# Kernel tuning notes

Hardware: AMD Instinct MI355X
Metric: run time of the kernel (lower is better)

## Reference

```python
import jax, jax.numpy as jnp
import numpy as np

B, R, N, K, E = 128, 500, 500, 10, 128
H1 = 5 * E  # UnvisitedMLP hidden = embedding_dim * 5


def setup_inputs() -> dict:
    key = jax.random.key(0)
    ks = jax.random.split(key, 8)
    current = jax.random.randint(ks[0], (B, R), 0, N)
    distance = jax.random.uniform(ks[1], (B, N, N), dtype=jnp.float32)
    # unvisited cities, exercising the padding-index path in search_unvisited.
    visited = jax.random.uniform(ks[2], (B, R, N)) < 0.97
    masked = jnp.where(visited, -jnp.inf, 0.0).astype(jnp.float32)
    encoded_nodes = jax.random.normal(ks[3], (B, N, E), dtype=jnp.float32)
    w1 = jax.random.normal(ks[4], (H1, K * E), dtype=jnp.float32) * (1.0 / np.sqrt(K * E))
    b1 = jnp.zeros((H1,), dtype=jnp.float32)
    w2 = jax.random.normal(ks[5], (E, H1), dtype=jnp.float32) * (1.0 / np.sqrt(H1))
    b2 = jnp.zeros((E,), dtype=jnp.float32)
    return {"current": current, "distance": distance, "masked": masked,
            "encoded_nodes": encoded_nodes, "w1": w1, "b1": b1, "w2": w2, "b2": b2}


def _search_unvisited(current, distance, masked, k_near):
    # distance_filtered[b, r, :] = distance[b, current[b, r], :]  -> [B, R, N]
    b_idx = jnp.arange(current.shape[0])[:, None]
    distance_filtered = distance[b_idx, current, :]
    mask_unvisited = masked != -jnp.inf
    distance_masked = jnp.where(mask_unvisited, distance_filtered, jnp.inf)
    # k smallest == top-k of negated distances
    neg_vals, k_idx = jax.lax.top_k(-distance_masked, k_near)  # [B, R, K]
    is_inf = neg_vals == -jnp.inf  # entries that were +inf (no unvisited left)
    n_cities = distance.shape[1]
    return jnp.where(is_inf, n_cities, k_idx)  # padding index = problem_size


def _gather_pad0(encoded_nodes, idx):
    # pad encoded_nodes with a zero row at index N, then gather  -> [B, R, K, E]
    padded = jnp.concatenate(
        [encoded_nodes, jnp.zeros_like(encoded_nodes[:, :1, :])], axis=1)
    b_idx = jnp.arange(encoded_nodes.shape[0])[:, None, None]
    return padded[b_idx, idx, :]


def _pad_avg(a):
    # replace all-zero (padding) rows along K with the mean of non-zero rows
    is_zero = a.sum(axis=-1) == 0  # [B, R, K]
    nz_count = jnp.clip((~is_zero).sum(axis=-1).astype(jnp.float32), 1e-9)
    mean_vec = a.sum(axis=2) / nz_count[..., None]  # [B, R, E]
    return jnp.where(is_zero[..., None], mean_vec[:, :, None, :], a)


def reference(current, distance, masked, encoded_nodes, w1, b1, w2, b2):
    k_near = K
    idx = _search_unvisited(current, distance, masked, k_near)  # [B, R, K]
    emb = _gather_pad0(encoded_nodes, idx)                      # [B, R, K, E]
    emb = _pad_avg(emb)
    h = emb.reshape(emb.shape[0], emb.shape[1], k_near * emb.shape[-1])  # [B, R, K*E]
    h = jax.nn.relu(jnp.einsum('brf,hf->brh', h, w1) + b1)
    out = jnp.einsum('brh,eh->bre', h, w2) + b2  # [B, R, E]
    return out
```

## Files before the change

### kernel.cpp

```cpp
#include <hip/hip_runtime.h>
#include <cstdint>
#include <cstddef>

#define Bn   128
#define Rn   500
#define Nn   500
#define Kn   10
#define En   128
#define H1n  640
#define KEn  1280
#define Mn   (Bn * Rn)

typedef short s16x8 __attribute__((ext_vector_type(8)));
typedef float f32x4 __attribute__((ext_vector_type(4)));

__device__ __forceinline__ unsigned short f2bf(float x) {
    union { float f; unsigned int u; } v; v.f = x;
    unsigned int r = v.u + 0x7fffu + ((v.u >> 16) & 1u);
    return (unsigned short)(r >> 16);
}
__device__ __forceinline__ float bf2f(unsigned short u) {
    union { unsigned int u; float f; } v; v.u = ((unsigned int)u) << 16;
    return v.f;
}
__device__ __forceinline__ void gl2lds16(const void* g, void* l) {
    __builtin_amdgcn_global_load_lds(
        (const __attribute__((address_space(1))) unsigned int*)g,
        (__attribute__((address_space(3))) unsigned int*)l, 16, 0, 0);
}
__device__ __forceinline__ void drain_all() {
    asm volatile("s_waitcnt vmcnt(0) lgkmcnt(0)" ::: "memory");
}
#define WAITV(n) asm volatile("s_waitcnt vmcnt(" #n ")" ::: "memory")
__device__ __forceinline__ void pipe_barrier() {
    __builtin_amdgcn_s_barrier();
    asm volatile("" ::: "memory");
}

__global__ void convw_kernel(const float* __restrict__ enc, const float* __restrict__ w1,
                             const float* __restrict__ w2,
                             unsigned short* __restrict__ encb, unsigned short* __restrict__ w1b,
                             unsigned short* __restrict__ w2b) {
    int i = blockIdx.x * 256 + threadIdx.x;
    if (i < (Bn * Nn * En) / 4) {
        float4 v = ((const float4*)enc)[i];
        ushort4 o; o.x = f2bf(v.x); o.y = f2bf(v.y); o.z = f2bf(v.z); o.w = f2bf(v.w);
        ((ushort4*)encb)[i] = o;
    }
    if (i < (H1n * KEn) / 4) {
        float4 v = ((const float4*)w1)[i];
        ushort4 o; o.x = f2bf(v.x); o.y = f2bf(v.y); o.z = f2bf(v.z); o.w = f2bf(v.w);
        ((ushort4*)w1b)[i] = o;
    }
    if (i < (En * H1n) / 4) {
        float4 v = ((const float4*)w2)[i];
        ushort4 o; o.x = f2bf(v.x); o.y = f2bf(v.y); o.z = f2bf(v.z); o.w = f2bf(v.w);
        ((ushort4*)w2b)[i] = o;
    }
}

__global__ __launch_bounds__(256) void select_kernel(const int* __restrict__ current,
                            const float* __restrict__ distance,
                            const float* __restrict__ masked,
                            const unsigned short* __restrict__ encb,
                            int* __restrict__ idx_out,
                            unsigned short* __restrict__ meanbb) {
    const int row  = blockIdx.x * 4 + (threadIdx.x >> 6);
    const int lane = threadIdx.x & 63;
    const int b    = row / Rn;
    const int cur  = current[row];
    const unsigned int* drow = (const unsigned int*)(distance + ((size_t)b * Nn + cur) * Nn);
    const unsigned int* mrow = (const unsigned int*)(masked + (size_t)row * Nn);

    unsigned long long key[8];
#pragma unroll
    for (int i = 0; i < 8; ++i) {
        int nn = lane + 64 * i;
        unsigned int fb = 0x7F800000u;
        if (nn < Nn) {
            unsigned int m = mrow[nn];
            unsigned int d = drow[nn];
            fb = (m == 0xFF800000u) ? 0x7F800000u : d;
        }
        key[i] = ((unsigned long long)fb << 32) | (unsigned int)nn;
    }

    int ids[Kn];
    int myid = Nn;
#pragma unroll
    for (int it = 0; it < Kn; ++it) {
        unsigned long long bk = key[0];
#pragma unroll
        for (int i = 1; i < 8; ++i) bk = (key[i] < bk) ? key[i] : bk;
#pragma unroll
        for (int off = 1; off < 64; off <<= 1) {
            unsigned long long ok = __shfl_xor(bk, off);
            bk = (ok < bk) ? ok : bk;
        }
        const int wid = ((bk >> 32) == 0x7F800000u) ? Nn : (int)(bk & 0xffffffffu);
        ids[it] = wid;
        if (lane == it) myid = wid;
#pragma unroll
        for (int i = 0; i < 8; ++i)
            if (key[i] == bk) key[i] = 0x7F800000FFFFFFFFull;
    }
    if (lane < Kn) idx_out[row * Kn + lane] = myid;

    const unsigned int* encu = (const unsigned int*)(encb + (size_t)b * Nn * En);
    float s0 = 0.f, s1 = 0.f; int cnt = 0;
#pragma unroll
    for (int k = 0; k < Kn; ++k) {
        const int id = ids[k];
        if (id < Nn) {
            unsigned int u = encu[id * (En / 2) + lane];
            s0 += bf2f((unsigned short)(u & 0xffffu));
            s1 += bf2f((unsigned short)(u >> 16));
            cnt++;
        }
    }
    float m0 = 0.f, m1 = 0.f;
    if (cnt > 0) { m0 = s0 / (float)cnt; m1 = s1 / (float)cnt; }
    unsigned int packed = (unsigned int)f2bf(m0) | ((unsigned int)f2bf(m1) << 16);
    ((unsigned int*)meanbb)[(size_t)row * (En / 2) + lane] = packed;
}

__global__ __launch_bounds__(512, 2) void gemm1_kernel(
        const unsigned short* __restrict__ encb, const unsigned short* __restrict__ meanbb,
        const int* __restrict__ idxb, const unsigned short* __restrict__ w1b,
        const float* __restrict__ b1, unsigned short* __restrict__ hbuf) {
    extern __shared__ unsigned short lds[];
    unsigned short* const As = lds;
    unsigned short* const Bs = lds + 3 * 256 * 64;

    const int p  = blockIdx.x;
    const int x  = p & 7;
    const int rk = p >> 3;
    const int w  = (x < 2 ? x * 157 : 314 + (x - 2) * 156) + rk;
    const int row0 = (w / 5) * 256;
    const int h0   = (w % 5) * 128;

    const int t    = threadIdx.x;
    const int lane = t & 63;
    const int wave = t >> 6;
    const int ln15 = lane & 15;
    const int q4   = lane >> 4;
    const int wm4  = wave & 3;
    const int wn   = wave >> 2;

    const int rl8 = lane >> 3;
    const int sc8 = lane & 7;
    const int cof = (sc8 ^ rl8) * 8;

    const unsigned short* encBp[4];
    const unsigned short* meanRp[4];
    int grA[4];
#pragma unroll
    for (int s = 0; s < 4; ++s) {
        const int gr = row0 + s * 64 + wave * 8 + rl8;
        grA[s]    = gr;
        encBp[s]  = encb + (size_t)(gr / Rn) * Nn * En;
        meanRp[s] = meanbb + (size_t)gr * En + cof;
    }
    const unsigned short* w1Rp[2];
#pragma unroll
    for (int s = 0; s < 2; ++s)
        w1Rp[s] = w1b + (size_t)(h0 + s * 64 + wave * 8 + rl8) * KEn + cof;

    int idr[4][Kn];
#pragma unroll
    for (int s = 0; s < 4; ++s)
#pragma unroll
        for (int j = 0; j < Kn; ++j)
            idr[s][j] = idxb[grA[s] * Kn + j];
    WAITV(0);

    f32x4 acc[4][4];
#pragma unroll
    for (int i = 0; i < 4; ++i)
#pragma unroll
        for (int j = 0; j < 4; ++j)
            acc[i][j] = (f32x4){0.f, 0.f, 0.f, 0.f};

    auto stA = [&](int s, int j, int e0, int b) {
        const int id = idr[s][j];
        const unsigned short* src = (id < Nn)
            ? (encBp[s] + (size_t)id * En + e0 + cof)
            : (meanRp[s] + e0);
        gl2lds16(src, As + (size_t)b * (256 * 64) + (s * 64 + wave * 8) * 64);
    };
    auto stB = [&](int s, int kt, int b) {
        gl2lds16(w1Rp[s] + kt * 64, Bs + (size_t)b * (128 * 64) + (s * 64 + wave * 8) * 64);
    };
    auto bundle0 = [&](int kt, int b) {
        const int j = kt >> 1, e0 = (kt & 1) * 64;
        stA(0, j, e0, b); stA(1, j, e0, b); stB(0, kt, b);
    };
    auto bundle1 = [&](int kt, int b) {
        const int j = kt >> 1, e0 = (kt & 1) * 64;
        stA(2, j, e0, b); stA(3, j, e0, b); stB(1, kt, b);
    };

    bundle0(0, 0); bundle1(0, 0);
    bundle0(1, 1); bundle1(1, 1);
    WAITV(6);
    pipe_barrier();

    const int rA = wm4 * 64 + ln15;
    const int rB = wn  * 64 + ln15;
    const int s7 = ln15 & 7;
    const int sl0 = (q4 ^ s7) * 8;
    const int sl1 = ((4 + q4) ^ s7) * 8;

#define MFMA16(a, bvec, c) c = __builtin_amdgcn_mfma_f32_16x16x32_bf16(a, bvec, c, 0, 0, 0)

#pragma unroll
    for (int kt = 0; kt < 20; ++kt) {
        const int cb = kt % 3;
        const unsigned short* Ab = As + cb * (256 * 64);
        const unsigned short* Bb = Bs + cb * (128 * 64);
        s16x8 af0, af1, af2, af3, bq0, bq1;

        af0 = *(const s16x8*)(Ab + (rA +  0) * 64 + sl0);
        af1 = *(const s16x8*)(Ab + (rA + 16) * 64 + sl0);
        af2 = *(const s16x8*)(Ab + (rA + 32) * 64 + sl0);
        af3 = *(const s16x8*)(Ab + (rA + 48) * 64 + sl0);
        bq0 = *(const s16x8*)(Bb + (rB +  0) * 64 + sl0);
        bq1 = *(const s16x8*)(Bb + (rB + 16) * 64 + sl0);
        if (kt + 2 < 20) bundle0(kt + 2, (kt + 2) % 3);
        pipe_barrier();
        __builtin_amdgcn_s_setprio(1);
        MFMA16(af0, bq0, acc[0][0]); MFMA16(af1, bq0, acc[1][0]);
        MFMA16(af2, bq0, acc[2][0]); MFMA16(af3, bq0, acc[3][0]);
        MFMA16(af0, bq1, acc[0][1]); MFMA16(af1, bq1, acc[1][1]);
        MFMA16(af2, bq1, acc[2][1]); MFMA16(af3, bq1, acc[3][1]);
        __builtin_amdgcn_s_setprio(0);
        pipe_barrier();

        bq0 = *(const s16x8*)(Bb + (rB + 32) * 64 + sl0);
        bq1 = *(const s16x8*)(Bb + (rB + 48) * 64 + sl0);
        pipe_barrier();
        __builtin_amdgcn_s_setprio(1);
        MFMA16(af0, bq0, acc[0][2]); MFMA16(af1, bq0, acc[1][2]);
        MFMA16(af2, bq0, acc[2][2]); MFMA16(af3, bq0, acc[3][2]);
        MFMA16(af0, bq1, acc[0][3]); MFMA16(af1, bq1, acc[1][3]);
        MFMA16(af2, bq1, acc[2][3]); MFMA16(af3, bq1, acc[3][3]);
        __builtin_amdgcn_s_setprio(0);
        pipe_barrier();

        af0 = *(const s16x8*)(Ab + (rA +  0) * 64 + sl1);
        af1 = *(const s16x8*)(Ab + (rA + 16) * 64 + sl1);
        af2 = *(const s16x8*)(Ab + (rA + 32) * 64 + sl1);
        af3 = *(const s16x8*)(Ab + (rA + 48) * 64 + sl1);
        bq0 = *(const s16x8*)(Bb + (rB +  0) * 64 + sl1);
        bq1 = *(const s16x8*)(Bb + (rB + 16) * 64 + sl1);
        if (kt + 2 < 20) bundle1(kt + 2, (kt + 2) % 3);
        pipe_barrier();
        __builtin_amdgcn_s_setprio(1);
        MFMA16(af0, bq0, acc[0][0]); MFMA16(af1, bq0, acc[1][0]);
        MFMA16(af2, bq0, acc[2][0]); MFMA16(af3, bq0, acc[3][0]);
        MFMA16(af0, bq1, acc[0][1]); MFMA16(af1, bq1, acc[1][1]);
        MFMA16(af2, bq1, acc[2][1]); MFMA16(af3, bq1, acc[3][1]);
        __builtin_amdgcn_s_setprio(0);
        pipe_barrier();

        bq0 = *(const s16x8*)(Bb + (rB + 32) * 64 + sl1);
        bq1 = *(const s16x8*)(Bb + (rB + 48) * 64 + sl1);
        pipe_barrier();
        __builtin_amdgcn_s_setprio(1);
        MFMA16(af0, bq0, acc[0][2]); MFMA16(af1, bq0, acc[1][2]);
        MFMA16(af2, bq0, acc[2][2]); MFMA16(af3, bq0, acc[3][2]);
        MFMA16(af0, bq1, acc[0][3]); MFMA16(af1, bq1, acc[1][3]);
        MFMA16(af2, bq1, acc[2][3]); MFMA16(af3, bq1, acc[3][3]);
        __builtin_amdgcn_s_setprio(0);
        if (kt + 2 < 20)      { WAITV(6); }
        else if (kt + 1 < 20) { WAITV(0); }
        pipe_barrier();
    }
#undef MFMA16

#pragma unroll
    for (int i = 0; i < 4; ++i) {
#pragma unroll
        for (int jj = 0; jj < 4; ++jj) {
            const int h = h0 + wn * 64 + jj * 16 + ln15;
            const float bias = b1[h];
#pragma unroll
            for (int rg = 0; rg < 4; ++rg) {
                const int m = wm4 * 64 + i * 16 + q4 * 4 + rg;
                float vv = acc[i][jj][rg] + bias;
                vv = fmaxf(vv, 0.f);
                hbuf[(size_t)(row0 + m) * H1n + h] = f2bf(vv);
            }
        }
    }
}

__global__ __launch_bounds__(256, 4) void gemm2_kernel(
        const unsigned short* __restrict__ hbuf, const unsigned short* __restrict__ w2b,
        const float* __restrict__ b2, float* __restrict__ out) {
    __shared__ alignas(16) unsigned short As[2][128 * 32];
    __shared__ alignas(16) unsigned short Bs[2][128 * 32];

    const int row0 = blockIdx.x * 128;
    const int t    = threadIdx.x;
    const int lane = t & 63;
    const int wave = t >> 6;
    const int ln15 = lane & 15;
    const int q4   = lane >> 4;
    const int wm   = wave & 1;
    const int wn   = wave >> 1;

    const int rl   = lane >> 2;
    const int sc   = lane & 3;
    const int coff = (sc ^ (rl & 3)) * 8;

    const unsigned short* hrow[2];
    const unsigned short* w2row[2];
#pragma unroll
    for (int s = 0; s < 2; ++s) {
        const int lr = wave * 32 + s * 16 + rl;
        hrow[s]  = hbuf + (size_t)(row0 + lr) * H1n + coff;
        w2row[s] = w2b + (size_t)lr * H1n + coff;
    }

    f32x4 acc[4][4];
#pragma unroll
    for (int i = 0; i < 4; ++i)
#pragma unroll
        for (int j = 0; j < 4; ++j)
            acc[i][j] = (f32x4){0.f, 0.f, 0.f, 0.f};

    auto issue = [&](int itk, int pb) {
        const int kk0 = itk * 32;
#pragma unroll
        for (int s = 0; s < 2; ++s) {
            gl2lds16(hrow[s] + kk0, &As[pb][(wave * 32 + s * 16) * 32]);
            gl2lds16(w2row[s] + kk0, &Bs[pb][(wave * 32 + s * 16) * 32]);
        }
    };

    issue(0, 0);

    for (int itk = 0; itk < H1n / 32; ++itk) {
        const int cur = itk & 1;
        drain_all();
        __syncthreads();
        if (itk + 1 < H1n / 32) issue(itk + 1, cur ^ 1);
        s16x8 af[4], bf[4];
#pragma unroll
        for (int i = 0; i < 4; ++i) {
            const int r = wm * 64 + i * 16 + ln15;
            af[i] = *(const s16x8*)&As[cur][r * 32 + (q4 ^ (r & 3)) * 8];
        }
#pragma unroll
        for (int jj = 0; jj < 4; ++jj) {
            const int r = wn * 64 + jj * 16 + ln15;
            bf[jj] = *(const s16x8*)&Bs[cur][r * 32 + (q4 ^ (r & 3)) * 8];
        }
#pragma unroll
        for (int i = 0; i < 4; ++i)
#pragma unroll
            for (int jj = 0; jj < 4; ++jj)
                acc[i][jj] = __builtin_amdgcn_mfma_f32_16x16x32_bf16(af[i], bf[jj], acc[i][jj], 0, 0, 0);
    }

#pragma unroll
    for (int i = 0; i < 4; ++i) {
#pragma unroll
        for (int jj = 0; jj < 4; ++jj) {
            const int e = wn * 64 + jj * 16 + ln15;
            const float bias = b2[e];
#pragma unroll
            for (int rg = 0; rg < 4; ++rg) {
                const int m = wm * 64 + i * 16 + q4 * 4 + rg;
                out[(size_t)(row0 + m) * En + e] = acc[i][jj][rg] + bias;
            }
        }
    }
}

extern "C" void kernel_launch(void* const* d_in, const int* in_sizes, int n_in,
                              void* d_out, int out_size, void* d_ws, size_t ws_size,
                              hipStream_t stream) {
    const int*   current  = (const int*)d_in[0];
    const float* distance = (const float*)d_in[1];
    const float* masked   = (const float*)d_in[2];
    const float* encoded  = (const float*)d_in[3];
    const float* w1       = (const float*)d_in[4];
    const float* b1       = (const float*)d_in[5];
    const float* w2       = (const float*)d_in[6];
    const float* b2       = (const float*)d_in[7];
    float* out = (float*)d_out;

    char* ws = (char*)d_ws;
    const size_t OFF_IDX  = 0;
    const size_t OFF_ENCB = 2560000;
    const size_t OFF_MEAN = OFF_ENCB + 16384000;
    const size_t OFF_W1B  = OFF_MEAN + 16384000;
    const size_t OFF_W2B  = OFF_W1B + 1638400;
    const size_t OFF_H    = OFF_W2B + 163840;
    int*            idxb   = (int*)(ws + OFF_IDX);
    unsigned short* encb   = (unsigned short*)(ws + OFF_ENCB);
    unsigned short* meanbb = (unsigned short*)(ws + OFF_MEAN);
    unsigned short* w1b    = (unsigned short*)(ws + OFF_W1B);
    unsigned short* w2b    = (unsigned short*)(ws + OFF_W2B);
    unsigned short* hbuf   = (unsigned short*)(ws + OFF_H);

    static bool s_attr = false;
    if (!s_attr) {
        hipFuncSetAttribute(reinterpret_cast<const void*>(gemm1_kernel),
                            hipFuncAttributeMaxDynamicSharedMemorySize, 147456);
        s_attr = true;
    }

    convw_kernel<<<(Bn * Nn * En / 4 + 255) / 256, 256, 0, stream>>>(encoded, w1, w2, encb, w1b, w2b);
    select_kernel<<<Mn / 4, 256, 0, stream>>>(current, distance, masked, encb, idxb, meanbb);
    gemm1_kernel<<<1250, 512, 147456, stream>>>(encb, meanbb, idxb, w1b, b1, hbuf);
    gemm2_kernel<<<Mn / 128, 256, 0, stream>>>(hbuf, w2b, b2, out);
}
```

Baseline: 469.4 us.

## Halve gemm1 K-tile, stage indices in LDS, triple-buffer gemm2 pipeline

gemm1's K tile drops from 64 to 32, so LDS per block falls from 144KB to about 77KB. The per-thread index registers are replaced by a shared LDS index table, and launch bounds rise so two blocks can share a CU. gemm2 moves from a double-buffered loop that drains memory and syncs every iteration to a triple-buffered software pipeline with split A/B issue, matching gemm1's structure. The gain is occupancy and overlap, paid for with twice as many, smaller K steps in gemm1 and more waitcnt/barrier overhead per unit of work.

```diff
diff --git a/kernel.cpp b/kernel.cpp
--- a/kernel.cpp
+++ b/kernel.cpp
@@ -124,13 +124,14 @@
     ((unsigned int*)meanbb)[(size_t)row * (En / 2) + lane] = packed;
 }
 
-__global__ __launch_bounds__(512, 2) void gemm1_kernel(
+__global__ __launch_bounds__(512, 4) void gemm1_kernel(
         const unsigned short* __restrict__ encb, const unsigned short* __restrict__ meanbb,
         const int* __restrict__ idxb, const unsigned short* __restrict__ w1b,
         const float* __restrict__ b1, unsigned short* __restrict__ hbuf) {
     extern __shared__ unsigned short lds[];
-    unsigned short* const As = lds;
-    unsigned short* const Bs = lds + 3 * 256 * 64;
+    unsigned short* const As   = lds;
+    unsigned short* const Bs   = lds + 3 * 256 * 32;
+    unsigned short* const idxs = lds + 3 * 256 * 32 + 3 * 128 * 32;
 
     const int p  = blockIdx.x;
     const int x  = p & 7;
@@ -147,32 +148,25 @@
     const int wm4  = wave & 3;
     const int wn   = wave >> 2;
 
-    const int rl8 = lane >> 3;
-    const int sc8 = lane & 7;
-    const int cof = (sc8 ^ rl8) * 8;
-
-    const unsigned short* encBp[4];
-    const unsigned short* meanRp[4];
-    int grA[4];
-#pragma unroll
-    for (int s = 0; s < 4; ++s) {
-        const int gr = row0 + s * 64 + wave * 8 + rl8;
-        grA[s]    = gr;
-        encBp[s]  = encb + (size_t)(gr / Rn) * Nn * En;
-        meanRp[s] = meanbb + (size_t)gr * En + cof;
-    }
-    const unsigned short* w1Rp[2];
-#pragma unroll
-    for (int s = 0; s < 2; ++s)
-        w1Rp[s] = w1b + (size_t)(h0 + s * 64 + wave * 8 + rl8) * KEn + cof;
-
-    int idr[4][Kn];
-#pragma unroll
-    for (int s = 0; s < 4; ++s)
-#pragma unroll
-        for (int j = 0; j < Kn; ++j)
-            idr[s][j] = idxb[grA[s] * Kn + j];
-    WAITV(0);
+    for (int i = t; i < 256 * Kn; i += 512)
+        idxs[i] = (unsigned short)idxb[row0 * Kn + i];
+
+    const int rl   = lane >> 2;
+    const int sc   = lane & 3;
+    const int coff = (sc ^ (rl & 3)) * 8;
+
+    int lrowA[2];
+    const unsigned short* encB[2];
+    const unsigned short* meanR[2];
+#pragma unroll
+    for (int s = 0; s < 2; ++s) {
+        lrowA[s] = wave * 32 + s * 16 + rl;
+        const int gr = row0 + lrowA[s];
+        encB[s]  = encb + (size_t)(gr / Rn) * Nn * En;
+        meanR[s] = meanbb + (size_t)gr * En + coff;
+    }
+    const int lrowB = wave * 16 + rl;
+    const unsigned short* w1R = w1b + (size_t)(h0 + lrowB) * KEn + coff;
 
     f32x4 acc[4][4];
 #pragma unroll
@@ -181,52 +175,50 @@
         for (int j = 0; j < 4; ++j)
             acc[i][j] = (f32x4){0.f, 0.f, 0.f, 0.f};
 
-    auto stA = [&](int s, int j, int e0, int b) {
-        const int id = idr[s][j];
-        const unsigned short* src = (id < Nn)
-            ? (encBp[s] + (size_t)id * En + e0 + cof)
-            : (meanRp[s] + e0);
-        gl2lds16(src, As + (size_t)b * (256 * 64) + (s * 64 + wave * 8) * 64);
+    auto issueA = [&](int kt, int cb) {
+        const int j  = kt >> 2;
+        const int e0 = (kt & 3) * 32;
+#pragma unroll
+        for (int s = 0; s < 2; ++s) {
+            const int id = idxs[lrowA[s] * Kn + j];
+            const unsigned short* src = (id < Nn)
+                ? (encB[s] + (size_t)id * En + e0 + coff)
+                : (meanR[s] + e0);
+            gl2lds16(src, As + (size_t)cb * (256 * 32) + (wave * 32 + s * 16) * 32);
+        }
     };
-    auto stB = [&](int s, int kt, int b) {
-        gl2lds16(w1Rp[s] + kt * 64, Bs + (size_t)b * (128 * 64) + (s * 64 + wave * 8) * 64);
+    auto issueB = [&](int kt, int cb) {
+        gl2lds16(w1R + kt * 32, Bs + (size_t)cb * (128 * 32) + (wave * 16) * 32);
     };
-    auto bundle0 = [&](int kt, int b) {
-        const int j = kt >> 1, e0 = (kt & 1) * 64;
-        stA(0, j, e0, b); stA(1, j, e0, b); stB(0, kt, b);
-    };
-    auto bundle1 = [&](int kt, int b) {
-        const int j = kt >> 1, e0 = (kt & 1) * 64;
-        stA(2, j, e0, b); stA(3, j, e0, b); stB(1, kt, b);
-    };
-
-    bundle0(0, 0); bundle1(0, 0);
-    bundle0(1, 1); bundle1(1, 1);
-    WAITV(6);
+
+    drain_all();
+    __syncthreads();
+    issueA(0, 0); issueB(0, 0);
+    issueA(1, 1); issueB(1, 1);
+    WAITV(3);
     pipe_barrier();
 
-    const int rA = wm4 * 64 + ln15;
-    const int rB = wn  * 64 + ln15;
-    const int s7 = ln15 & 7;
-    const int sl0 = (q4 ^ s7) * 8;
-    const int sl1 = ((4 + q4) ^ s7) * 8;
+    const int rA  = wm4 * 64 + ln15;
+    const int rB  = wn  * 64 + ln15;
+    const int slA = (q4 ^ (rA & 3)) * 8;
+    const int slB = (q4 ^ (rB & 3)) * 8;
 
 #define MFMA16(a, bvec, c) c = __builtin_amdgcn_mfma_f32_16x16x32_bf16(a, bvec, c, 0, 0, 0)
 
 #pragma unroll
-    for (int kt = 0; kt < 20; ++kt) {
+    for (int kt = 0; kt < 40; ++kt) {
         const int cb = kt % 3;
-        const unsigned short* Ab = As + cb * (256 * 64);
-        const unsigned short* Bb = Bs + cb * (128 * 64);
+        const unsigned short* Ab = As + cb * (256 * 32);
+        const unsigned short* Bb = Bs + cb * (128 * 32);
         s16x8 af0, af1, af2, af3, bq0, bq1;
 
-        af0 = *(const s16x8*)(Ab + (rA +  0) * 64 + sl0);
-        af1 = *(const s16x8*)(Ab + (rA + 16) * 64 + sl0);
-        af2 = *(const s16x8*)(Ab + (rA + 32) * 64 + sl0);
-        af3 = *(const s16x8*)(Ab + (rA + 48) * 64 + sl0);
-        bq0 = *(const s16x8*)(Bb + (rB +  0) * 64 + sl0);
-        bq1 = *(const s16x8*)(Bb + (rB + 16) * 64 + sl0);
-        if (kt + 2 < 20) bundle0(kt + 2, (kt + 2) % 3);
+        af0 = *(const s16x8*)(Ab + (rA +  0) * 32 + slA);
+        af1 = *(const s16x8*)(Ab + (rA + 16) * 32 + slA);
+        af2 = *(const s16x8*)(Ab + (rA + 32) * 32 + slA);
+        af3 = *(const s16x8*)(Ab + (rA + 48) * 32 + slA);
+        bq0 = *(const s16x8*)(Bb + (rB +  0) * 32 + slB);
+        bq1 = *(const s16x8*)(Bb + (rB + 16) * 32 + slB);
+        if (kt + 2 < 40) issueA(kt + 2, (kt + 2) % 3);
         pipe_barrier();
         __builtin_amdgcn_s_setprio(1);
         MFMA16(af0, bq0, acc[0][0]); MFMA16(af1, bq0, acc[1][0]);
@@ -236,8 +228,9 @@
         __builtin_amdgcn_s_setprio(0);
         pipe_barrier();
 
-        bq0 = *(const s16x8*)(Bb + (rB + 32) * 64 + sl0);
-        bq1 = *(const s16x8*)(Bb + (rB + 48) * 64 + sl0);
+        bq0 = *(const s16x8*)(Bb + (rB + 32) * 32 + slB);
+        bq1 = *(const s16x8*)(Bb + (rB + 48) * 32 + slB);
+        if (kt + 2 < 40) issueB(kt + 2, (kt + 2) % 3);
         pipe_barrier();
         __builtin_amdgcn_s_setprio(1);
         MFMA16(af0, bq0, acc[0][2]); MFMA16(af1, bq0, acc[1][2]);
@@ -245,35 +238,8 @@
         MFMA16(af0, bq1, acc[0][3]); MFMA16(af1, bq1, acc[1][3]);
         MFMA16(af2, bq1, acc[2][3]); MFMA16(af3, bq1, acc[3][3]);
         __builtin_amdgcn_s_setprio(0);
-        pipe_barrier();
-
-        af0 = *(const s16x8*)(Ab + (rA +  0) * 64 + sl1);
-        af1 = *(const s16x8*)(Ab + (rA + 16) * 64 + sl1);
-        af2 = *(const s16x8*)(Ab + (rA + 32) * 64 + sl1);
-        af3 = *(const s16x8*)(Ab + (rA + 48) * 64 + sl1);
-        bq0 = *(const s16x8*)(Bb + (rB +  0) * 64 + sl1);
-        bq1 = *(const s16x8*)(Bb + (rB + 16) * 64 + sl1);
-        if (kt + 2 < 20) bundle1(kt + 2, (kt + 2) % 3);
-        pipe_barrier();
-        __builtin_amdgcn_s_setprio(1);
-        MFMA16(af0, bq0, acc[0][0]); MFMA16(af1, bq0, acc[1][0]);
-        MFMA16(af2, bq0, acc[2][0]); MFMA16(af3, bq0, acc[3][0]);
-        MFMA16(af0, bq1, acc[0][1]); MFMA16(af1, bq1, acc[1][1]);
-        MFMA16(af2, bq1, acc[2][1]); MFMA16(af3, bq1, acc[3][1]);
-        __builtin_amdgcn_s_setprio(0);
-        pipe_barrier();
-
-        bq0 = *(const s16x8*)(Bb + (rB + 32) * 64 + sl1);
-        bq1 = *(const s16x8*)(Bb + (rB + 48) * 64 + sl1);
-        pipe_barrier();
-        __builtin_amdgcn_s_setprio(1);
-        MFMA16(af0, bq0, acc[0][2]); MFMA16(af1, bq0, acc[1][2]);
-        MFMA16(af2, bq0, acc[2][2]); MFMA16(af3, bq0, acc[3][2]);
-        MFMA16(af0, bq1, acc[0][3]); MFMA16(af1, bq1, acc[1][3]);
-        MFMA16(af2, bq1, acc[2][3]); MFMA16(af3, bq1, acc[3][3]);
-        __builtin_amdgcn_s_setprio(0);
-        if (kt + 2 < 20)      { WAITV(6); }
-        else if (kt + 1 < 20) { WAITV(0); }
+        if (kt + 2 < 40)      { WAITV(3); }
+        else if (kt + 1 < 40) { WAITV(0); }
         pipe_barrier();
     }
 #undef MFMA16
@@ -298,8 +264,8 @@
 __global__ __launch_bounds__(256, 4) void gemm2_kernel(
         const unsigned short* __restrict__ hbuf, const unsigned short* __restrict__ w2b,
         const float* __restrict__ b2, float* __restrict__ out) {
-    __shared__ alignas(16) unsigned short As[2][128 * 32];
-    __shared__ alignas(16) unsigned short Bs[2][128 * 32];
+    __shared__ alignas(16) unsigned short As[3][128 * 32];
+    __shared__ alignas(16) unsigned short Bs[3][128 * 32];
 
     const int row0 = blockIdx.x * 128;
     const int t    = threadIdx.x;
@@ -330,39 +296,67 @@
         for (int j = 0; j < 4; ++j)
             acc[i][j] = (f32x4){0.f, 0.f, 0.f, 0.f};
 
-    auto issue = [&](int itk, int pb) {
-        const int kk0 = itk * 32;
-#pragma unroll
-        for (int s = 0; s < 2; ++s) {
-            gl2lds16(hrow[s] + kk0, &As[pb][(wave * 32 + s * 16) * 32]);
-            gl2lds16(w2row[s] + kk0, &Bs[pb][(wave * 32 + s * 16) * 32]);
-        }
+    auto issueA = [&](int kt, int cb) {
+#pragma unroll
+        for (int s = 0; s < 2; ++s)
+            gl2lds16(hrow[s] + kt * 32, &As[cb][(wave * 32 + s * 16) * 32]);
     };
-
-    issue(0, 0);
-
-    for (int itk = 0; itk < H1n / 32; ++itk) {
-        const int cur = itk & 1;
-        drain_all();
-        __syncthreads();
-        if (itk + 1 < H1n / 32) issue(itk + 1, cur ^ 1);
-        s16x8 af[4], bf[4];
-#pragma unroll
-        for (int i = 0; i < 4; ++i) {
-            const int r = wm * 64 + i * 16 + ln15;
-            af[i] = *(const s16x8*)&As[cur][r * 32 + (q4 ^ (r & 3)) * 8];
-        }
-#pragma unroll
-        for (int jj = 0; jj < 4; ++jj) {
-            const int r = wn * 64 + jj * 16 + ln15;
-            bf[jj] = *(const s16x8*)&Bs[cur][r * 32 + (q4 ^ (r & 3)) * 8];
-        }
-#pragma unroll
-        for (int i = 0; i < 4; ++i)
-#pragma unroll
-            for (int jj = 0; jj < 4; ++jj)
-                acc[i][jj] = __builtin_amdgcn_mfma_f32_16x16x32_bf16(af[i], bf[jj], acc[i][jj], 0, 0, 0);
-    }
+    auto issueB = [&](int kt, int cb) {
+#pragma unroll
+        for (int s = 0; s < 2; ++s)
+            gl2lds16(w2row[s] + kt * 32, &Bs[cb][(wave * 32 + s * 16) * 32]);
+    };
+
+    issueA(0, 0); issueB(0, 0);
+    issueA(1, 1); issueB(1, 1);
+    WAITV(4);
+    pipe_barrier();
+
+    const int rA  = wm * 64 + ln15;
+    const int rB  = wn * 64 + ln15;
+    const int slA = (q4 ^ (rA & 3)) * 8;
+    const int slB = (q4 ^ (rB & 3)) * 8;
+
+#define MFMA16(a, bvec, c) c = __builtin_amdgcn_mfma_f32_16x16x32_bf16(a, bvec, c, 0, 0, 0)
+
+#pragma unroll
+    for (int kt = 0; kt < 20; ++kt) {
+        const int cb = kt % 3;
+        const unsigned short* Ab = As[cb];
+        const unsigned short* Bb = Bs[cb];
+        s16x8 af0, af1, af2, af3, bq0, bq1;
+
+        af0 = *(const s16x8*)(Ab + (rA +  0) * 32 + slA);
+        af1 = *(const s16x8*)(Ab + (rA + 16) * 32 + slA);
+        af2 = *(const s16x8*)(Ab + (rA + 32) * 32 + slA);
+        af3 = *(const s16x8*)(Ab + (rA + 48) * 32 + slA);
+        bq0 = *(const s16x8*)(Bb + (rB +  0) * 32 + slB);
+        bq1 = *(const s16x8*)(Bb + (rB + 16) * 32 + slB);
+        if (kt + 2 < 20) issueA(kt + 2, (kt + 2) % 3);
+        pipe_barrier();
+        __builtin_amdgcn_s_setprio(1);
+        MFMA16(af0, bq0, acc[0][0]); MFMA16(af1, bq0, acc[1][0]);
+        MFMA16(af2, bq0, acc[2][0]); MFMA16(af3, bq0, acc[3][0]);
+        MFMA16(af0, bq1, acc[0][1]); MFMA16(af1, bq1, acc[1][1]);
+        MFMA16(af2, bq1, acc[2][1]); MFMA16(af3, bq1, acc[3][1]);
+        __builtin_amdgcn_s_setprio(0);
+        pipe_barrier();
+
+        bq0 = *(const s16x8*)(Bb + (rB + 32) * 32 + slB);
+        bq1 = *(const s16x8*)(Bb + (rB + 48) * 32 + slB);
+        if (kt + 2 < 20) issueB(kt + 2, (kt + 2) % 3);
+        pipe_barrier();
+        __builtin_amdgcn_s_setprio(1);
+        MFMA16(af0, bq0, acc[0][2]); MFMA16(af1, bq0, acc[1][2]);
+        MFMA16(af2, bq0, acc[2][2]); MFMA16(af3, bq0, acc[3][2]);
+        MFMA16(af0, bq1, acc[0][3]); MFMA16(af1, bq1, acc[1][3]);
+        MFMA16(af2, bq1, acc[2][3]); MFMA16(af3, bq1, acc[3][3]);
+        __builtin_amdgcn_s_setprio(0);
+        if (kt + 2 < 20)      { WAITV(4); }
+        else if (kt + 1 < 20) { WAITV(0); }
+        pipe_barrier();
+    }
+#undef MFMA16
 
 #pragma unroll
     for (int i = 0; i < 4; ++i) {
@@ -409,12 +403,12 @@
     static bool s_attr = false;
     if (!s_attr) {
         hipFuncSetAttribute(reinterpret_cast<const void*>(gemm1_kernel),
-                            hipFuncAttributeMaxDynamicSharedMemorySize, 147456);
+                            hipFuncAttributeMaxDynamicSharedMemorySize, 78848);
         s_attr = true;
     }
 
     convw_kernel<<<(Bn * Nn * En / 4 + 255) / 256, 256, 0, stream>>>(encoded, w1, w2, encb, w1b, w2b);
     select_kernel<<<Mn / 4, 256, 0, stream>>>(current, distance, masked, encb, idxb, meanbb);
-    gemm1_kernel<<<1250, 512, 147456, stream>>>(encb, meanbb, idxb, w1b, b1, hbuf);
+    gemm1_kernel<<<1250, 512, 78848, stream>>>(encb, meanbb, idxb, w1b, b1, hbuf);
     gemm2_kernel<<<Mn / 128, 256, 0, stream>>>(hbuf, w2b, b2, out);
 }
```

New measurement: 467.5 us. Within noise of the previous version (-0.4%).
